# Kernel tuning notes

Measured on AMD Instinct MI355X. Metric: run time of the kernel, lower is better.

Reference implementation:

```python
import jax, jax.numpy as jnp
import numpy as np

IMG = 224          # mask height/width, hardcoded in the module
OUT = 256          # Linear(224*224 -> 256)
BOX = 20           # half-width of the square mask around the farthest joint


def setup_inputs() -> dict:
    key = jax.random.key(0)
    k1, k2, k3, k4 = jax.random.split(key, 4)
    B, J, T = 256, 25, 64
    rgbfuture = jax.random.normal(k1, (B, OUT), dtype=jnp.float32)
    # normalized joint coords kept in [0.1, 0.9] so pixel_x in [22, 201] (original
    # code has no x-clamping and would hit numpy negative-slice wraparound otherwise)
    skeleton_future = 0.1 + 0.8 * jax.random.uniform(k2, (B, J, T, 3), dtype=jnp.float32)
    W = jax.random.normal(k3, (OUT, IMG * IMG), dtype=jnp.float32) / np.sqrt(IMG * IMG)
    b = jax.random.normal(k4, (OUT,), dtype=jnp.float32) * 0.01
    return {"rgbfuture": rgbfuture, "skeleton_future": skeleton_future, "W": W, "b": b}


def reference(rgbfuture, skeleton_future, W, b):
    B, J, T, _ = skeleton_future.shape
    mid = J // 2

    # distance of every joint trajectory to the middle joint, per frame: [B, J, T]
    diff = skeleton_future - skeleton_future[:, mid:mid + 1]
    dist = jnp.linalg.norm(diff, axis=-1)
    t_max = jnp.argmax(dist, axis=-1)                       # [B, J]

    # farthest-frame coordinates per joint: [B, J, 3]
    pts = jnp.take_along_axis(skeleton_future, t_max[:, :, None, None], axis=2)[:, :, 0, :]
    px = (pts[..., 0] * IMG).astype(jnp.int32)              # int() truncation == floor (positive)
    py = (pts[..., 1] * IMG).astype(jnp.int32)

    rows = jnp.arange(IMG)
    # x-range: [px-20, px+20) (inputs guarantee in-frame)
    xm = (rows >= (px - BOX)[..., None]) & (rows < (px + BOX)[..., None])   # [B, J, IMG]
    # y-range with the module's explicit edge handling
    y_lo = jnp.where(py < BOX, 0, py - BOX)
    y_hi = jnp.where(py > IMG - BOX, IMG, py + BOX)
    ym = (rows >= y_lo[..., None]) & (rows < y_hi[..., None])               # [B, J, IMG]

    keep = jnp.arange(J) != mid                              # middle joint is skipped
    box = xm[:, :, :, None] & ym[:, :, None, :] & keep[None, :, None, None]  # [B, J, IMG, IMG]
    mask = jnp.any(box, axis=1).astype(rgbfuture.dtype)      # torch.max over joints == union

    merged = mask.reshape(B, IMG * IMG) @ W.T + b            # [B, 256]
    return rgbfuture * merged
```

## Files before the change

### kernel.cpp

```cpp
#include <hip/hip_runtime.h>
#include <hip/hip_bf16.h>
#include <stdint.h>

#define IMG   224
#define OUTD  256
#define BATCH 256
#define JD    25
#define TD    64
#define MIDJ  12
#define BOXR  20

#define OFF_RUNS 25804800u
#define OFF_PART 33144832u
#define OFF_CNT  35241984u

__global__ void k_wpref(const float* __restrict__ W, __hip_bfloat16* __restrict__ P) {
    const int x  = blockIdx.x;
    const int o0 = blockIdx.y * 32;
    const int tid = threadIdx.x;

    __shared__ float lds[32][225];
    __shared__ float carry[8][32];

    #pragma unroll
    for (int it = 0; it < 28; ++it) {
        const int k = it * 256 + tid;
        const int r = k / 224;
        const int y = k - r * 224;
        lds[r][y] = W[(size_t)(o0 + r) * (IMG * IMG) + (size_t)x * IMG + y];
    }
    __syncthreads();

    const int ol  = tid & 31;
    const int seg = tid >> 5;
    const int y0  = seg * 28;

    float ssum = 0.0f;
    #pragma unroll
    for (int i = 0; i < 28; ++i) ssum += lds[ol][y0 + i];
    carry[seg][ol] = ssum;
    __syncthreads();

    float s = 0.0f;
    for (int s2 = 0; s2 < seg; ++s2) s += carry[s2][ol];

    __hip_bfloat16* p = P + ((size_t)x * 225) * 256 + o0 + ol;
    if (seg == 0) p[0] = __float2bfloat16(0.0f);
    #pragma unroll
    for (int i = 0; i < 28; ++i) {
        s += lds[ol][y0 + i];
        p[(size_t)(y0 + i + 1) * 256] = __float2bfloat16(s);
    }
}

__global__ void k_boxes_runs(const float* __restrict__ skel, uint32_t* __restrict__ runs,
                             uint8_t* __restrict__ cnt) {
    const int b = blockIdx.x;
    const int wave = threadIdx.x >> 6;
    const int t = threadIdx.x & 63;
    __shared__ int s_px[JD], s_ylo[JD], s_yhi[JD];

    const float* sb = skel + (size_t)b * JD * TD * 3;
    const float mx = sb[(MIDJ * TD + t) * 3 + 0];
    const float my = sb[(MIDJ * TD + t) * 3 + 1];
    const float mz = sb[(MIDJ * TD + t) * 3 + 2];

    for (int j = wave; j < JD; j += 4) {
        const float ax = sb[(j * TD + t) * 3 + 0];
        const float ay = sb[(j * TD + t) * 3 + 1];
        const float az = sb[(j * TD + t) * 3 + 2];
        const float dx = ax - mx, dy = ay - my, dz = az - mz;
        const float d2 = __fadd_rn(__fadd_rn(__fmul_rn(dx, dx), __fmul_rn(dy, dy)),
                                   __fmul_rn(dz, dz));
        float bd = sqrtf(d2);
        int   bi = t;
        #pragma unroll
        for (int off = 1; off < 64; off <<= 1) {
            const float od = __shfl_xor(bd, off);
            const int   oi = __shfl_xor(bi, off);
            if (od > bd || (od == bd && oi < bi)) { bd = od; bi = oi; }
        }
        if (t == 0) {
            const float ptx = sb[(j * TD + bi) * 3 + 0];
            const float pty = sb[(j * TD + bi) * 3 + 1];
            const int px = (int)(ptx * 224.0f);
            const int py = (int)(pty * 224.0f);
            s_px[j]  = px;
            s_ylo[j] = (py < BOXR) ? 0 : (py - BOXR);
            s_yhi[j] = (py > IMG - BOXR) ? IMG : (py + BOXR);
        }
    }
    __syncthreads();

    const int x = threadIdx.x;
    if (x >= IMG) return;

    unsigned long long m0 = 0, m1 = 0, m2 = 0, m3 = 0;
    for (int j = 0; j < JD; ++j) {
        if (j == MIDJ) continue;
        const int px = s_px[j];
        if (x >= px - BOXR && x < px + BOXR) {
            const int lo = s_ylo[j], hi = s_yhi[j];
            auto setw = [&](unsigned long long& mw, int wbase) {
                int l = lo - wbase; int h = hi - wbase;
                l = l < 0 ? 0 : l; h = h > 64 ? 64 : h;
                if (l < h) {
                    unsigned long long msk =
                        (h - l == 64) ? ~0ull : ((((1ull << (h - l)) - 1ull)) << l);
                    mw |= msk;
                }
            };
            setw(m0, 0); setw(m1, 64); setw(m2, 128); setw(m3, 192);
        }
    }

    uint32_t* rb = runs + ((size_t)b * IMG + x) * 32;
    int n = 0, start = -1;
    auto scanw = [&](unsigned long long bits, int wbase) {
        int pos = 0;
        while (pos < 64) {
            if (start < 0) {
                const unsigned long long tt = bits >> pos;
                if (!tt) return;
                pos += __builtin_ctzll(tt);
                start = wbase + pos;
            } else {
                const unsigned long long tt = (~bits) >> pos;
                if (!tt) return;
                pos += __builtin_ctzll(tt);
                rb[n] = (uint32_t)start | ((uint32_t)(wbase + pos) << 8);
                ++n; start = -1;
            }
        }
    };
    scanw(m0, 0); scanw(m1, 64); scanw(m2, 128); scanw(m3, 192);
    if (start >= 0) { rb[n] = (uint32_t)start | (224u << 8); ++n; }
    cnt[(size_t)b * IMG + x] = (uint8_t)n;
}

__global__ void k_accum(const uint32_t* __restrict__ runs,
                        const uint8_t* __restrict__ cnt,
                        const uint32_t* __restrict__ P32,
                        float* __restrict__ part) {
    const int b = blockIdx.x >> 3;
    const int s = blockIdx.x & 7;
    const int tid = threadIdx.x;
    const int x0 = s * 28;

    __shared__ uint8_t  scnt[28];
    __shared__ uint16_t soff[29];
    __shared__ uint32_t slist[28 * 12];

    if (tid < 28) scnt[tid] = cnt[(size_t)b * IMG + x0 + tid];
    __syncthreads();
    if (tid == 0) {
        uint16_t acc = 0;
        #pragma unroll
        for (int i = 0; i < 28; ++i) { soff[i] = acc; acc += scnt[i]; }
        soff[28] = acc;
    }
    __syncthreads();

    for (int e = tid; e < 28 * 12; e += 128) {
        const int xl = e / 12;
        const int j  = e - xl * 12;
        if (j < (int)scnt[xl]) {
            const uint32_t raw = runs[((size_t)b * IMG + x0 + xl) * 32 + j];
            slist[soff[xl] + j] = raw | ((uint32_t)xl << 17);
        }
    }
    __syncthreads();

    const int total = soff[28];
    float a0 = 0.0f, a1 = 0.0f;
    for (int i = 0; i < total; ++i) {
        const uint32_t e = slist[i];
        const int xl = (int)(e >> 17);
        const int a  = (int)(e & 255u);
        const int c  = (int)((e >> 8) & 511u);
        const uint32_t* px = P32 + (size_t)(x0 + xl) * 225 * 128 + tid;
        const uint32_t va = px[(size_t)a * 128];
        const uint32_t vc = px[(size_t)c * 128];
        a0 += __uint_as_float(vc << 16) - __uint_as_float(va << 16);
        a1 += __uint_as_float(vc & 0xffff0000u) - __uint_as_float(va & 0xffff0000u);
    }

    float* pp = part + (((size_t)b * 8 + s) * 256) + (size_t)tid * 2;
    pp[0] = a0;
    pp[1] = a1;
}

__global__ void k_final(const float* __restrict__ rgb, const float* __restrict__ bias,
                        const float* __restrict__ part, float* __restrict__ out) {
    const int idx = blockIdx.x * 256 + threadIdx.x;
    const int b = idx >> 8, o = idx & 255;
    float m = bias[o];
    #pragma unroll
    for (int s = 0; s < 8; ++s) m += part[(((size_t)b * 8 + s) * 256) + o];
    out[idx] = rgb[idx] * m;
}

extern "C" void kernel_launch(void* const* d_in, const int* in_sizes, int n_in,
                              void* d_out, int out_size, void* d_ws, size_t ws_size,
                              hipStream_t stream) {
    const float* rgb  = (const float*)d_in[0];
    const float* skel = (const float*)d_in[1];
    const float* W    = (const float*)d_in[2];
    const float* bias = (const float*)d_in[3];
    float* out = (float*)d_out;

    uint8_t* ws = (uint8_t*)d_ws;
    __hip_bfloat16* P = (__hip_bfloat16*)(ws);
    uint32_t* runs = (uint32_t*)(ws + OFF_RUNS);
    float* part = (float*)(ws + OFF_PART);
    uint8_t* cnt = (uint8_t*)(ws + OFF_CNT);

    k_wpref<<<dim3(IMG, 8), dim3(256), 0, stream>>>(W, P);
    k_boxes_runs<<<dim3(BATCH), dim3(256), 0, stream>>>(skel, runs, cnt);
    k_accum<<<dim3(BATCH * 8), dim3(128), 0, stream>>>(runs, cnt, (const uint32_t*)P, part);
    k_final<<<dim3(BATCH), dim3(256), 0, stream>>>(rgb, bias, part, out);
}
```

Measured before the change: 48.16 us.

## Fuse W prefix-sum and box-run kernels into one launch with XCD-aware mapping

Merges the W prefix-sum kernel and the skeleton box/run extraction kernel into one launch. The first 1792 blocks do the prefix sums and the remaining 256 do the boxes, so both run concurrently and one launch is saved. Block IDs are remapped so that each XCD handles a contiguous range of x columns, W is read with nontemporal loads, and the accumulation loop is unrolled by two with independent accumulators to overlap gathers. The fused kernel carries the union of both shared-memory footprints, which may reduce occupancy for the smaller box blocks.

Result: faster. 45.43 us (-5.7%).

```diff
diff --git a/kernel.cpp b/kernel.cpp
--- a/kernel.cpp
+++ b/kernel.cpp
@@ -14,51 +14,61 @@
 #define OFF_PART 33144832u
 #define OFF_CNT  35241984u
 
-__global__ void k_wpref(const float* __restrict__ W, __hip_bfloat16* __restrict__ P) {
-    const int x  = blockIdx.x;
-    const int o0 = blockIdx.y * 32;
+
+__global__ void KA(const float* __restrict__ W, __hip_bfloat16* __restrict__ P,
+                   const float* __restrict__ skel, uint32_t* __restrict__ runs,
+                   uint8_t* __restrict__ cnt) {
+    const int id  = blockIdx.x;
     const int tid = threadIdx.x;
 
     __shared__ float lds[32][225];
     __shared__ float carry[8][32];
-
-    #pragma unroll
-    for (int it = 0; it < 28; ++it) {
-        const int k = it * 256 + tid;
-        const int r = k / 224;
-        const int y = k - r * 224;
-        lds[r][y] = W[(size_t)(o0 + r) * (IMG * IMG) + (size_t)x * IMG + y];
-    }
-    __syncthreads();
-
-    const int ol  = tid & 31;
-    const int seg = tid >> 5;
-    const int y0  = seg * 28;
-
-    float ssum = 0.0f;
-    #pragma unroll
-    for (int i = 0; i < 28; ++i) ssum += lds[ol][y0 + i];
-    carry[seg][ol] = ssum;
-    __syncthreads();
-
-    float s = 0.0f;
-    for (int s2 = 0; s2 < seg; ++s2) s += carry[s2][ol];
-
-    __hip_bfloat16* p = P + ((size_t)x * 225) * 256 + o0 + ol;
-    if (seg == 0) p[0] = __float2bfloat16(0.0f);
-    #pragma unroll
-    for (int i = 0; i < 28; ++i) {
-        s += lds[ol][y0 + i];
-        p[(size_t)(y0 + i + 1) * 256] = __float2bfloat16(s);
-    }
-}
-
-__global__ void k_boxes_runs(const float* __restrict__ skel, uint32_t* __restrict__ runs,
-                             uint8_t* __restrict__ cnt) {
-    const int b = blockIdx.x;
-    const int wave = threadIdx.x >> 6;
-    const int t = threadIdx.x & 63;
     __shared__ int s_px[JD], s_ylo[JD], s_yhi[JD];
+
+    if (id < 1792) {
+        const int xcd = id & 7;
+        const int g   = id >> 3;
+        const int oc  = g & 7;
+        const int xi  = g >> 3;
+        const int x   = xcd * 28 + xi;
+        const int o0  = oc * 32;
+
+        #pragma unroll
+        for (int it = 0; it < 28; ++it) {
+            const int k = it * 256 + tid;
+            const int r = k / 224;
+            const int y = k - r * 224;
+            lds[r][y] = __builtin_nontemporal_load(
+                &W[(size_t)(o0 + r) * (IMG * IMG) + (size_t)x * IMG + y]);
+        }
+        __syncthreads();
+
+        const int ol  = tid & 31;
+        const int seg = tid >> 5;
+        const int y0  = seg * 28;
+
+        float ssum = 0.0f;
+        #pragma unroll
+        for (int i = 0; i < 28; ++i) ssum += lds[ol][y0 + i];
+        carry[seg][ol] = ssum;
+        __syncthreads();
+
+        float s = 0.0f;
+        for (int s2 = 0; s2 < seg; ++s2) s += carry[s2][ol];
+
+        __hip_bfloat16* p = P + ((size_t)x * 225) * 256 + o0 + ol;
+        if (seg == 0) p[0] = __float2bfloat16(0.0f);
+        #pragma unroll
+        for (int i = 0; i < 28; ++i) {
+            s += lds[ol][y0 + i];
+            p[(size_t)(y0 + i + 1) * 256] = __float2bfloat16(s);
+        }
+        return;
+    }
+
+    const int b = id - 1792;
+    const int wave = tid >> 6;
+    const int t = tid & 63;
 
     const float* sb = skel + (size_t)b * JD * TD * 3;
     const float mx = sb[(MIDJ * TD + t) * 3 + 0];
@@ -92,7 +102,7 @@
     }
     __syncthreads();
 
-    const int x = threadIdx.x;
+    const int x = tid;
     if (x >= IMG) return;
 
     unsigned long long m0 = 0, m1 = 0, m2 = 0, m3 = 0;
@@ -172,22 +182,35 @@
     __syncthreads();
 
     const int total = soff[28];
-    float a0 = 0.0f, a1 = 0.0f;
-    for (int i = 0; i < total; ++i) {
-        const uint32_t e = slist[i];
-        const int xl = (int)(e >> 17);
-        const int a  = (int)(e & 255u);
-        const int c  = (int)((e >> 8) & 511u);
-        const uint32_t* px = P32 + (size_t)(x0 + xl) * 225 * 128 + tid;
-        const uint32_t va = px[(size_t)a * 128];
-        const uint32_t vc = px[(size_t)c * 128];
-        a0 += __uint_as_float(vc << 16) - __uint_as_float(va << 16);
-        a1 += __uint_as_float(vc & 0xffff0000u) - __uint_as_float(va & 0xffff0000u);
+    const uint32_t* Pbase = P32 + (size_t)x0 * 225 * 128 + tid;
+    float a0 = 0.0f, a1 = 0.0f, b0 = 0.0f, b1 = 0.0f;
+    int i = 0;
+    for (; i + 2 <= total; i += 2) {
+        const uint32_t e0 = slist[i];
+        const uint32_t e1 = slist[i + 1];
+        const uint32_t* px0 = Pbase + (size_t)(e0 >> 17) * (225 * 128);
+        const uint32_t* px1 = Pbase + (size_t)(e1 >> 17) * (225 * 128);
+        const uint32_t va0 = px0[(size_t)(e0 & 255u) * 128];
+        const uint32_t vc0 = px0[(size_t)((e0 >> 8) & 511u) * 128];
+        const uint32_t va1 = px1[(size_t)(e1 & 255u) * 128];
+        const uint32_t vc1 = px1[(size_t)((e1 >> 8) & 511u) * 128];
+        a0 += __uint_as_float(vc0 << 16) - __uint_as_float(va0 << 16);
+        a1 += __uint_as_float(vc0 & 0xffff0000u) - __uint_as_float(va0 & 0xffff0000u);
+        b0 += __uint_as_float(vc1 << 16) - __uint_as_float(va1 << 16);
+        b1 += __uint_as_float(vc1 & 0xffff0000u) - __uint_as_float(va1 & 0xffff0000u);
+    }
+    if (i < total) {
+        const uint32_t e0 = slist[i];
+        const uint32_t* px0 = Pbase + (size_t)(e0 >> 17) * (225 * 128);
+        const uint32_t va0 = px0[(size_t)(e0 & 255u) * 128];
+        const uint32_t vc0 = px0[(size_t)((e0 >> 8) & 511u) * 128];
+        a0 += __uint_as_float(vc0 << 16) - __uint_as_float(va0 << 16);
+        a1 += __uint_as_float(vc0 & 0xffff0000u) - __uint_as_float(va0 & 0xffff0000u);
     }
 
     float* pp = part + (((size_t)b * 8 + s) * 256) + (size_t)tid * 2;
-    pp[0] = a0;
-    pp[1] = a1;
+    pp[0] = a0 + b0;
+    pp[1] = a1 + b1;
 }
 
 __global__ void k_final(const float* __restrict__ rgb, const float* __restrict__ bias,
@@ -215,8 +238,7 @@
     float* part = (float*)(ws + OFF_PART);
     uint8_t* cnt = (uint8_t*)(ws + OFF_CNT);
 
-    k_wpref<<<dim3(IMG, 8), dim3(256), 0, stream>>>(W, P);
-    k_boxes_runs<<<dim3(BATCH), dim3(256), 0, stream>>>(skel, runs, cnt);
+    KA<<<dim3(2048), dim3(256), 0, stream>>>(W, P, skel, runs, cnt);
     k_accum<<<dim3(BATCH * 8), dim3(128), 0, stream>>>(runs, cnt, (const uint32_t*)P, part);
     k_final<<<dim3(BATCH), dim3(256), 0, stream>>>(rgb, bias, part, out);
 }
```
